# Optimization experiments

Hardware: AMD Instinct MI355X
Metric: run time of the kernel (lower is better)

Reference implementation:

```python
import jax, jax.numpy as jnp
import numpy as np

CHUNK = 16

def setup_inputs() -> dict:
    key = jax.random.key(0)
    k1, k2, k3, k4 = jax.random.split(key, 4)
    B, T, D, N = 2, 2048, 1024, 16
    u_input = jax.random.normal(k1, (B, T, D), dtype=jnp.float32)
    delta = jax.random.uniform(k2, (B, T, D), dtype=jnp.float32)
    b_mat = jax.random.normal(k3, (B, T, D, N), dtype=jnp.float32)
    c_mat = jax.random.normal(k4, (B, T, D, N), dtype=jnp.float32)
    A_log = jnp.log(jnp.linspace(1.0, float(N), N)).astype(jnp.float32)
    return {"u_input": u_input, "delta": delta, "b_mat": b_mat, "c_mat": c_mat, "A_log": A_log}

def reference(u_input, delta, b_mat, c_mat, A_log):
    B, T, D = u_input.shape
    N = A_log.shape[0]
    L = min(CHUNK, T)
    C = T // L  # T chosen divisible by chunk size
    A = -jnp.exp(A_log)  # [N], broadcasts over [B,L,D,N]

    # reshape into chunks and move chunk axis first for lax.scan
    u_c = jnp.moveaxis(u_input.reshape(B, C, L, D), 1, 0)       # [C,B,L,D]
    d_c = jnp.moveaxis(delta.reshape(B, C, L, D), 1, 0)        # [C,B,L,D]
    b_c = jnp.moveaxis(b_mat.reshape(B, C, L, D, N), 1, 0)     # [C,B,L,D,N]
    c_c = jnp.moveaxis(c_mat.reshape(B, C, L, D, N), 1, 0)     # [C,B,L,D,N]

    def step(h, inp):
        u, dl, b, c = inp  # u,dl: [B,L,D]; b,c: [B,L,D,N]; h: [B,D,N]
        deltaA = jnp.clip(dl[..., None] * A, -10.0, 10.0)      # [B,L,D,N]
        eA = jnp.exp(deltaA)
        frac = jnp.where(jnp.abs(deltaA) < 1e-4,
                         dl[..., None],
                         (eA - 1.0) / (A + 1e-12))
        Bu = frac * (b * u[..., None])                          # [B,L,D,N]
        Ah_cum = jnp.cumprod(eA, axis=1)
        h_expand = h[:, None] * Ah_cum                          # [B,L,D,N]
        # flip_weights[t] = eA[t] for t < L-1, and 1 at t = L-1
        fw = jnp.concatenate([eA[:, :-1], jnp.ones_like(eA[:, :1])], axis=1)
        Bu_term = jnp.flip(jnp.cumsum(Bu * fw, axis=1), axis=1)
        h_new = h_expand + Bu_term
        y = (h_new * c).sum(-1)                                 # [B,L,D]
        return h_new[:, -1], y

    h0 = jnp.zeros((B, D, N), dtype=u_input.dtype)
    _, ys = jax.lax.scan(step, h0, (u_c, d_c, b_c, c_c))        # ys: [C,B,L,D]
    return jnp.moveaxis(ys, 0, 1).reshape(B, T, D)
```

## Files before the change

kernel.cpp:

```cpp
#include <hip/hip_runtime.h>

#define BB 2
#define TT 2048
#define DD 1024
#define NN 16
#define LL 16
#define CC (TT / LL)

__global__ __launch_bounds__(256) void k1a_segxform(
    const float* __restrict__ delta,
    const float* __restrict__ u,
    const float* __restrict__ bmat,
    const float* __restrict__ A_log,
    float* __restrict__ Pseg,
    float* __restrict__ Qseg,
    int S, int CPS)
{
    int g = blockIdx.x * 256 + threadIdx.x;
    int n   = g & (NN - 1);
    int d   = (g >> 4) & (DD - 1);
    int seg = (g >> 14) & (S - 1);
    int b   = g >> (14 + 5);

    float A_n  = -__expf(A_log[n]);
    float rinv = 1.0f / (A_n + 1e-12f);

    float P = 1.0f, Q = 0.0f;
    int c0 = seg * CPS;
    for (int c = c0; c < c0 + CPS; ++c) {
        int t0 = c * LL;
        int base = (b * TT + t0) * DD + d;

        float dl[LL];
        #pragma unroll
        for (int t = 0; t < LL; ++t) dl[t] = delta[base + t * DD];
        float bm0 = bmat[base * NN + n];
        float uu0 = u[base];

        float p = 1.0f;
        float q = 0.0f;
        #pragma unroll
        for (int t = 0; t < LL; ++t) {
            float dA = fminf(fmaxf(dl[t] * A_n, -10.0f), 10.0f);
            float eA = __expf(dA);
            if (t == 0) {
                float frac = (fabsf(dA) < 1e-4f) ? dl[t] : (eA - 1.0f) * rinv;
                q = frac * (bm0 * uu0) * eA;
            }
            p *= eA;
        }
        P = P * p;
        Q = Q * p + q;
    }
    Pseg[g] = P;
    Qseg[g] = Q;
}

__global__ __launch_bounds__(256) void k1b_scan(
    const float* __restrict__ Pseg,
    const float* __restrict__ Qseg,
    float* __restrict__ hin,
    int S)
{
    int g = blockIdx.x * 256 + threadIdx.x;
    int dn = g & (DD * NN - 1);
    int b  = g >> 14;

    float h = 0.0f;
    for (int s = 0; s < S; ++s) {
        int idx = (b * S + s) * (DD * NN) + dn;
        hin[idx] = h;
        h = h * Pseg[idx] + Qseg[idx];
    }
}

__global__ __launch_bounds__(256) void k2_main(
    const float* __restrict__ delta,
    const float* __restrict__ u,
    const float* __restrict__ bmat,
    const float* __restrict__ cmat,
    const float* __restrict__ A_log,
    const float* __restrict__ hin,
    float* __restrict__ out,
    int S, int CPS)
{
    const int dblks = DD / 16;
    int blocks_per_b = S * dblks;
    int b   = blockIdx.x / blocks_per_b;
    int r   = blockIdx.x - b * blocks_per_b;
    int seg = r / dblks;
    int dblk = r - seg * dblks;

    int n = threadIdx.x & 15;
    int d = dblk * 16 + (threadIdx.x >> 4);

    float A_n  = -__expf(A_log[n]);
    float rinv = 1.0f / (A_n + 1e-12f);

    float h = hin[((b * S + seg) * DD + d) * NN + n];
    int t0seg = seg * (TT / S);

    for (int c = 0; c < CPS; ++c) {
        int t0 = t0seg + c * LL;
        int base = (b * TT + t0) * DD + d;

        float dl[LL], bu[LL], cm[LL];
        #pragma unroll
        for (int t = 0; t < LL; ++t) {
            int bt = base + t * DD;
            dl[t] = delta[bt];
            float uu = u[bt];
            float bm = bmat[bt * NN + n];
            cm[t] = cmat[bt * NN + n];
            bu[t] = bm * uu;
        }

        float cp[LL], pref[LL];
        float prun = 1.0f, srun = 0.0f;
        #pragma unroll
        for (int t = 0; t < LL; ++t) {
            float dA = fminf(fmaxf(dl[t] * A_n, -10.0f), 10.0f);
            float eA = __expf(dA);
            float frac = (fabsf(dA) < 1e-4f) ? dl[t] : (eA - 1.0f) * rinv;
            float Bu = frac * bu[t];
            float gg = Bu * ((t < LL - 1) ? eA : 1.0f);
            prun *= eA;
            cp[t] = prun;
            srun += gg;
            pref[t] = srun;
        }

        float yv = 0.0f;
        #pragma unroll
        for (int t = 0; t < LL; ++t) {
            float hn = h * cp[t] + pref[LL - 1 - t];
            float v  = hn * cm[t];
            v += __shfl_xor(v, 1);
            v += __shfl_xor(v, 2);
            v += __shfl_xor(v, 4);
            v += __shfl_xor(v, 8);
            if (n == t) yv = v;
        }
        h = h * cp[LL - 1] + pref[0];

        out[base + n * DD] = yv;
    }
}

extern "C" void kernel_launch(void* const* d_in, const int* in_sizes, int n_in,
                              void* d_out, int out_size, void* d_ws, size_t ws_size,
                              hipStream_t stream) {
    (void)in_sizes; (void)n_in; (void)out_size;

    const float* u     = (const float*)d_in[0];
    const float* delta = (const float*)d_in[1];
    const float* bmat  = (const float*)d_in[2];
    const float* cmat  = (const float*)d_in[3];
    const float* A_log = (const float*)d_in[4];
    float* out = (float*)d_out;

    const int S = 32;
    const int CPS = CC / S;

    size_t tbl = (size_t)BB * S * DD * NN;
    float* Pseg = (float*)d_ws;
    float* Qseg = Pseg + tbl;
    float* hin  = Qseg + tbl;
    (void)ws_size;

    k1a_segxform<<<(BB * S * DD * NN) / 256, 256, 0, stream>>>(
        delta, u, bmat, A_log, Pseg, Qseg, S, CPS);
    k1b_scan<<<(BB * DD * NN) / 256, 256, 0, stream>>>(Pseg, Qseg, hin, S);
    k2_main<<<BB * S * (DD / 16), 256, 0, stream>>>(
        delta, u, bmat, cmat, A_log, hin, out, S, CPS);
}
```

Before: 600.4 us.

## Process two state channels per thread with float2 loads in scan kernels

Each thread in the segment-transform and main kernels now handles two of the sixteen state channels, loading b and c as float2 and writing segment tables as float2. This halves the thread count and the redundant per-thread loads of delta and u, and the shuffle reduction drops one step. The main kernel also fuses the load and exponent loops and writes output directly from one lane per group, dropping the per-lane select. Segment count and chunks-per-segment become compile-time constants and launch bounds gain an occupancy hint. The cost is more registers per thread and fewer threads to hide memory latency.

```diff
diff --git a/kernel.cpp b/kernel.cpp
--- a/kernel.cpp
+++ b/kernel.cpp
@@ -6,54 +6,61 @@
 #define NN 16
 #define LL 16
 #define CC (TT / LL)
+#define SS 32
+#define CPS (CC / SS)
 
-__global__ __launch_bounds__(256) void k1a_segxform(
+__global__ __launch_bounds__(256, 4) void k1a_segxform(
     const float* __restrict__ delta,
     const float* __restrict__ u,
     const float* __restrict__ bmat,
     const float* __restrict__ A_log,
     float* __restrict__ Pseg,
-    float* __restrict__ Qseg,
-    int S, int CPS)
+    float* __restrict__ Qseg)
 {
-    int g = blockIdx.x * 256 + threadIdx.x;
-    int n   = g & (NN - 1);
-    int d   = (g >> 4) & (DD - 1);
-    int seg = (g >> 14) & (S - 1);
-    int b   = g >> (14 + 5);
+    int g   = blockIdx.x * 256 + threadIdx.x;
+    int ng  = g & 7;
+    int d   = (g >> 3) & (DD - 1);
+    int seg = (g >> 13) & (SS - 1);
+    int b   = g >> 18;
+    int n0  = ng * 2;
 
-    float A_n  = -__expf(A_log[n]);
-    float rinv = 1.0f / (A_n + 1e-12f);
+    float A0 = -__expf(A_log[n0]);
+    float A1 = -__expf(A_log[n0 + 1]);
+    float r0 = 1.0f / (A0 + 1e-12f);
+    float r1 = 1.0f / (A1 + 1e-12f);
 
-    float P = 1.0f, Q = 0.0f;
-    int c0 = seg * CPS;
-    for (int c = c0; c < c0 + CPS; ++c) {
-        int t0 = c * LL;
+    float P0 = 1.0f, P1 = 1.0f, Q0 = 0.0f, Q1 = 0.0f;
+    int t0seg = seg * (TT / SS);
+    for (int c = 0; c < CPS; ++c) {
+        int t0   = t0seg + c * LL;
         int base = (b * TT + t0) * DD + d;
 
         float dl[LL];
         #pragma unroll
         for (int t = 0; t < LL; ++t) dl[t] = delta[base + t * DD];
-        float bm0 = bmat[base * NN + n];
-        float uu0 = u[base];
+        float  uu0 = u[base];
+        float2 bv  = *reinterpret_cast<const float2*>(&bmat[(long)base * NN + n0]);
 
-        float p = 1.0f;
-        float q = 0.0f;
+        float p0 = 1.0f, p1 = 1.0f, q0 = 0.0f, q1 = 0.0f;
         #pragma unroll
         for (int t = 0; t < LL; ++t) {
-            float dA = fminf(fmaxf(dl[t] * A_n, -10.0f), 10.0f);
-            float eA = __expf(dA);
+            float dA0 = fminf(fmaxf(dl[t] * A0, -10.0f), 10.0f);
+            float dA1 = fminf(fmaxf(dl[t] * A1, -10.0f), 10.0f);
+            float e0 = __expf(dA0), e1 = __expf(dA1);
             if (t == 0) {
-                float frac = (fabsf(dA) < 1e-4f) ? dl[t] : (eA - 1.0f) * rinv;
-                q = frac * (bm0 * uu0) * eA;
+                float f0 = (fabsf(dA0) < 1e-4f) ? dl[t] : (e0 - 1.0f) * r0;
+                float f1 = (fabsf(dA1) < 1e-4f) ? dl[t] : (e1 - 1.0f) * r1;
+                q0 = f0 * (bv.x * uu0) * e0;
+                q1 = f1 * (bv.y * uu0) * e1;
             }
-            p *= eA;
+            p0 *= e0; p1 *= e1;
         }
-        P = P * p;
-        Q = Q * p + q;
+        P0 *= p0; Q0 = Q0 * p0 + q0;
+        P1 *= p1; Q1 = Q1 * p1 + q1;
     }
-    Pseg[g] = P;
-    Qseg[g] = Q;
+    int oidx = ((b * SS + seg) * DD + d) * NN + n0;
+    *reinterpret_cast<float2*>(&Pseg[oidx]) = make_float2(P0, P1);
+    *reinterpret_cast<float2*>(&Qseg[oidx]) = make_float2(Q0, Q1);
 }
 
 __global__ __launch_bounds__(256) void k1b_scan(
@@ -62,7 +69,7 @@
     float* __restrict__ hin,
     int S)
 {
-    int g = blockIdx.x * 256 + threadIdx.x;
+    int g  = blockIdx.x * 256 + threadIdx.x;
     int dn = g & (DD * NN - 1);
     int b  = g >> 14;
 
@@ -74,83 +81,83 @@
     }
 }
 
-__global__ __launch_bounds__(256) void k2_main(
+__global__ __launch_bounds__(256, 4) void k2_main(
     const float* __restrict__ delta,
     const float* __restrict__ u,
     const float* __restrict__ bmat,
     const float* __restrict__ cmat,
     const float* __restrict__ A_log,
     const float* __restrict__ hin,
-    float* __restrict__ out,
-    int S, int CPS)
+    float* __restrict__ out)
 {
-    const int dblks = DD / 16;
-    int blocks_per_b = S * dblks;
-    int b   = blockIdx.x / blocks_per_b;
-    int r   = blockIdx.x - b * blocks_per_b;
-    int seg = r / dblks;
-    int dblk = r - seg * dblks;
+    int g   = blockIdx.x * 256 + threadIdx.x;
+    int ng  = g & 7;
+    int d   = (g >> 3) & (DD - 1);
+    int seg = (g >> 13) & (SS - 1);
+    int b   = g >> 18;
+    int n0  = ng * 2;
 
-    int n = threadIdx.x & 15;
-    int d = dblk * 16 + (threadIdx.x >> 4);
+    float A0 = -__expf(A_log[n0]);
+    float A1 = -__expf(A_log[n0 + 1]);
+    float r0 = 1.0f / (A0 + 1e-12f);
+    float r1 = 1.0f / (A1 + 1e-12f);
 
-    float A_n  = -__expf(A_log[n]);
-    float rinv = 1.0f / (A_n + 1e-12f);
+    float2 hv = *reinterpret_cast<const float2*>(
+        &hin[((b * SS + seg) * DD + d) * NN + n0]);
+    float h0 = hv.x, h1 = hv.y;
 
-    float h = hin[((b * S + seg) * DD + d) * NN + n];
-    int t0seg = seg * (TT / S);
+    int t0seg = seg * (TT / SS);
+    for (int c = 0; c < CPS; ++c) {
+        int  t0    = t0seg + c * LL;
+        int  base  = (b * TT + t0) * DD + d;
+        long nbase = (long)base * NN + n0;
 
-    for (int c = 0; c < CPS; ++c) {
-        int t0 = t0seg + c * LL;
-        int base = (b * TT + t0) * DD + d;
-
-        float dl[LL], bu[LL], cm[LL];
+        float cp0[LL], cp1[LL], g0[LL], g1[LL];
+        float pr0 = 1.0f, pr1 = 1.0f;
         #pragma unroll
         for (int t = 0; t < LL; ++t) {
-            int bt = base + t * DD;
-            dl[t] = delta[bt];
-            float uu = u[bt];
-            float bm = bmat[bt * NN + n];
-            cm[t] = cmat[bt * NN + n];
-            bu[t] = bm * uu;
+            float  dlv = delta[base + t * DD];
+            float  uv  = u[base + t * DD];
+            float2 bv  = *reinterpret_cast<const float2*>(
+                &bmat[nbase + (long)t * (DD * NN)]);
+            float dA0 = fminf(fmaxf(dlv * A0, -10.0f), 10.0f);
+            float dA1 = fminf(fmaxf(dlv * A1, -10.0f), 10.0f);
+            float e0 = __expf(dA0), e1 = __expf(dA1);
+            float f0 = (fabsf(dA0) < 1e-4f) ? dlv : (e0 - 1.0f) * r0;
+            float f1 = (fabsf(dA1) < 1e-4f) ? dlv : (e1 - 1.0f) * r1;
+            float Bu0 = f0 * (bv.x * uv);
+            float Bu1 = f1 * (bv.y * uv);
+            pr0 *= e0; pr1 *= e1;
+            cp0[t] = pr0; cp1[t] = pr1;
+            g0[t] = Bu0 * ((t < LL - 1) ? e0 : 1.0f);
+            g1[t] = Bu1 * ((t < LL - 1) ? e1 : 1.0f);
         }
 
-        float cp[LL], pref[LL];
-        float prun = 1.0f, srun = 0.0f;
+        float cs0 = 0.0f, cs1 = 0.0f;
         #pragma unroll
-        for (int t = 0; t < LL; ++t) {
-            float dA = fminf(fmaxf(dl[t] * A_n, -10.0f), 10.0f);
-            float eA = __expf(dA);
-            float frac = (fabsf(dA) < 1e-4f) ? dl[t] : (eA - 1.0f) * rinv;
-            float Bu = frac * bu[t];
-            float gg = Bu * ((t < LL - 1) ? eA : 1.0f);
-            prun *= eA;
-            cp[t] = prun;
-            srun += gg;
-            pref[t] = srun;
-        }
-
-        float yv = 0.0f;
-        #pragma unroll
-        for (int t = 0; t < LL; ++t) {
-            float hn = h * cp[t] + pref[LL - 1 - t];
-            float v  = hn * cm[t];
+        for (int k = 0; k < LL; ++k) {
+            int t = LL - 1 - k;
+            cs0 += g0[k];
+            cs1 += g1[k];
+            float2 cv = *reinterpret_cast<const float2*>(
+                &cmat[nbase + (long)t * (DD * NN)]);
+            float v = cv.x * (h0 * cp0[t] + cs0)
+                    + cv.y * (h1 * cp1[t] + cs1);
             v += __shfl_xor(v, 1);
             v += __shfl_xor(v, 2);
             v += __shfl_xor(v, 4);
-            v += __shfl_xor(v, 8);
-            if (n == t) yv = v;
+            if (ng == 0) out[base + t * DD] = v;
         }
-        h = h * cp[LL - 1] + pref[0];
 
-        out[base + n * DD] = yv;
+        h0 = h0 * cp0[LL - 1] + g0[0];
+        h1 = h1 * cp1[LL - 1] + g1[0];
     }
 }
 
 extern "C" void kernel_launch(void* const* d_in, const int* in_sizes, int n_in,
                               void* d_out, int out_size, void* d_ws, size_t ws_size,
                               hipStream_t stream) {
-    (void)in_sizes; (void)n_in; (void)out_size;
+    (void)in_sizes; (void)n_in; (void)out_size; (void)ws_size;
 
     const float* u     = (const float*)d_in[0];
     const float* delta = (const float*)d_in[1];
@@ -159,18 +166,14 @@
     const float* A_log = (const float*)d_in[4];
     float* out = (float*)d_out;
 
-    const int S = 32;
-    const int CPS = CC / S;
-
-    size_t tbl = (size_t)BB * S * DD * NN;
+    size_t tbl = (size_t)BB * SS * DD * NN;
     float* Pseg = (float*)d_ws;
     float* Qseg = Pseg + tbl;
     float* hin  = Qseg + tbl;
-    (void)ws_size;
 
-    k1a_segxform<<<(BB * S * DD * NN) / 256, 256, 0, stream>>>(
-        delta, u, bmat, A_log, Pseg, Qseg, S, CPS);
-    k1b_scan<<<(BB * DD * NN) / 256, 256, 0, stream>>>(Pseg, Qseg, hin, S);
-    k2_main<<<BB * S * (DD / 16), 256, 0, stream>>>(
-        delta, u, bmat, cmat, A_log, hin, out, S, CPS);
+    k1a_segxform<<<(BB * SS * DD * (NN / 2)) / 256, 256, 0, stream>>>(
+        delta, u, bmat, A_log, Pseg, Qseg);
+    k1b_scan<<<(BB * DD * NN) / 256, 256, 0, stream>>>(Pseg, Qseg, hin, SS);
+    k2_main<<<(BB * SS * DD * (NN / 2)) / 256, 256, 0, stream>>>(
+        delta, u, bmat, cmat, A_log, hin, out);
 }
```

Result: slower. 681.8 us (+13.6%).
